# Optimization experiments

Hardware: AMD Instinct MI355X
Metric: run time of the kernel (lower is better)

## Reference

```python
import jax, jax.numpy as jnp
import numpy as np

ARITY, LABEL_DIM, H_DIM, B = 2, 128, 512, 16384
ARG_DIM = LABEL_DIM + ARITY * H_DIM


def setup_inputs() -> dict:
    key = jax.random.key(0)
    ks = jax.random.split(key, 12)
    s_lin = 1.0 / np.sqrt(ARG_DIM)
    inp = {
        "label": jax.random.normal(ks[0], (B, LABEL_DIM), jnp.float32),
        "children_h": jax.random.normal(ks[1], (ARITY, B, H_DIM), jnp.float32),
        "children_c": jax.random.normal(ks[2], (ARITY, B, H_DIM), jnp.float32),
        # torch Linear params: W (h, arg_dim), b (h,)
        "W_i": jax.random.normal(ks[3], (H_DIM, ARG_DIM), jnp.float32) * s_lin,
        "b_i": jax.random.normal(ks[4], (H_DIM,), jnp.float32) * s_lin,
        "W_o": jax.random.normal(ks[5], (H_DIM, ARG_DIM), jnp.float32) * s_lin,
        "b_o": jax.random.normal(ks[6], (H_DIM,), jnp.float32) * s_lin,
        "W_u": jax.random.normal(ks[7], (H_DIM, ARG_DIM), jnp.float32) * s_lin,
        "b_u": jax.random.normal(ks[8], (H_DIM,), jnp.float32) * s_lin,
        # forget params (xavier-ish init)
        "W_fl": jax.random.normal(ks[9], (H_DIM, LABEL_DIM), jnp.float32) * np.sqrt(2.0 / (H_DIM + LABEL_DIM)),
        "W_fs": jax.random.normal(ks[10], (ARITY, ARITY, H_DIM, H_DIM), jnp.float32) * np.sqrt(1.0 / H_DIM),
        "forget_bias": jax.random.normal(ks[11], (H_DIM,), jnp.float32) * 0.1,
    }
    return inp


def reference(label, children_h, children_c, W_i, b_i, W_o, b_o, W_u, b_u, W_fl, W_fs, forget_bias):
    arity, b, h = children_h.shape
    # x = cat([label, h_0, ..., h_{arity-1}], dim=1)  -> (B, arg_dim)
    x = jnp.concatenate([label, children_h.transpose(1, 0, 2).reshape(b, arity * h)], axis=1)
    i_gate = jax.nn.sigmoid(x @ W_i.T + b_i)
    o_gate = jax.nn.sigmoid(x @ W_o.T + b_o)
    u = jnp.tanh(x @ W_u.T + b_u)
    # per-child forget weight: [W_fl | W_fs[k,0] | ... | W_fs[k,arity-1]]  -> (arity, h, arg_dim)
    Wf = jnp.concatenate(
        [jnp.broadcast_to(W_fl, (arity,) + W_fl.shape),
         W_fs.transpose(0, 2, 1, 3).reshape(arity, h, arity * h)],
        axis=2,
    )
    # bmm (no bias inside sigmoid; forget_bias enters separately below)
    f = jax.nn.sigmoid(jnp.einsum("khd,bd->kbh", Wf, x))
    cells_composed = (f * children_c).sum(axis=0)          # (B, h)
    cells_forget_bias = forget_bias * children_c.sum(axis=0)
    next_cell = i_gate * u + cells_composed + cells_forget_bias
    out = jnp.tanh(o_gate * next_cell)
    return (next_cell, out)
```

## Files before the change

kernel.cpp:

```cpp
#include <hip/hip_runtime.h>
#include <hip/hip_bf16.h>
#include <cstdint>
#include <cstddef>

#define BROWS   16384
#define LDIM    128
#define HDIM    512
#define KDIM    1152
#define NGATES  2560
#define NKT     (KDIM / 64)

#define XB_BYTES  ((size_t)BROWS * KDIM * 2)
#define WB_BYTES  ((size_t)NGATES * KDIM * 2)

using f32x4   = __attribute__((ext_vector_type(4))) float;
using bfrag   = __attribute__((ext_vector_type(8))) short;

__device__ __forceinline__ short f2bf(float f) {
    union { float f; uint32_t u; } a; a.f = f;
    uint32_t u = a.u;
    uint32_t lsb = (u >> 16) & 1u;
    u += 0x7fffu + lsb;
    return (short)(u >> 16);
}

__device__ __forceinline__ void load_lds16(const void* g, void* l) {
    __builtin_amdgcn_global_load_lds(
        (const __attribute__((address_space(1))) void*)g,
        (__attribute__((address_space(3))) void*)l, 16, 0, 0);
}

__device__ __forceinline__ float fast_sigmoid(float x) {
    return 1.0f / (1.0f + __expf(-x));
}
__device__ __forceinline__ float fast_tanh(float x) {
    float t = __expf(2.0f * x);
    return 1.0f - 2.0f / (t + 1.0f);
}

#define NBX  ((BROWS  * (KDIM / 8)) / 256)
#define NBW  ((NGATES * (KDIM / 8)) / 256)

__global__ __launch_bounds__(256) void pack_all(
    const float* __restrict__ label, const float* __restrict__ chh,
    const float* __restrict__ Wi, const float* __restrict__ Wo,
    const float* __restrict__ Wu, const float* __restrict__ Wfl,
    const float* __restrict__ Wfs,
    short* __restrict__ xb, short* __restrict__ Wb)
{
    const int perRow = KDIM / 8;
    int blk = blockIdx.x;
    const float* src;
    short* dst;
    if (blk < NBX) {
        int tid = blk * 256 + threadIdx.x;
        int b = tid / perRow;
        int d = (tid - b * perRow) * 8;
        if (d < LDIM) {
            src = label + (size_t)b * LDIM + d;
        } else {
            int dd = d - LDIM;
            int k  = dd >> 9;
            int j  = dd & 511;
            src = chh + ((size_t)k * BROWS + b) * HDIM + j;
        }
        dst = xb + (size_t)b * KDIM + d;
    } else {
        int tid = (blk - NBX) * 256 + threadIdx.x;
        int n = tid / perRow;
        int d = (tid - n * perRow) * 8;
        int g = n >> 9, h = n & 511;
        if (g == 0)      src = Wi + (size_t)h * KDIM + d;
        else if (g == 1) src = Wo + (size_t)h * KDIM + d;
        else if (g == 2) src = Wu + (size_t)h * KDIM + d;
        else {
            int k = g - 3;
            if (d < LDIM) {
                src = Wfl + (size_t)h * LDIM + d;
            } else {
                int dd = d - LDIM;
                int j  = dd >> 9;
                int jj = dd & 511;
                src = Wfs + (((size_t)(k * 2 + j) * HDIM + h) * HDIM) + jj;
            }
        }
        dst = Wb + (size_t)n * KDIM + d;
    }
    float4 v0 = *(const float4*)src;
    float4 v1 = *(const float4*)(src + 4);
    bfrag s;
    s[0] = f2bf(v0.x); s[1] = f2bf(v0.y); s[2] = f2bf(v0.z); s[3] = f2bf(v0.w);
    s[4] = f2bf(v1.x); s[5] = f2bf(v1.y); s[6] = f2bf(v1.z); s[7] = f2bf(v1.w);
    *(bfrag*)dst = s;
}

__global__ __launch_bounds__(512, 2) void gemm_fused(
    const short* __restrict__ A, const short* __restrict__ Wb,
    const float* __restrict__ chc,
    const float* __restrict__ b_i, const float* __restrict__ b_o,
    const float* __restrict__ b_u, const float* __restrict__ fbias,
    float* __restrict__ out)
{
    __shared__ short As[2][16384];
    __shared__ short Bs[2][20480];

    const int t    = threadIdx.x;
    const int lane = t & 63;
    const int wave = t >> 6;
    const int wr   = wave >> 2;
    const int wc   = wave & 3;
    const int quad = lane >> 4;
    const int l16  = lane & 15;

    const int local = blockIdx.x >> 3;
    const int mT    = (blockIdx.x & 7) * 8 + (local >> 3);
    const int nT    = local & 7;
    const int mBase = mT * 256;
    const int h0    = nT * 64;

    f32x4 acc[8][5] = {};

    const int sr  = t >> 3;
    const int ssl = (t & 7) ^ (sr & 7);
    const short* aSrc = A  + (size_t)(mBase + sr) * KDIM + ssl * 8;
    const short* bSrc = Wb + (size_t)(h0    + sr) * KDIM + ssl * 8;
    short* aDst = &As[0][0] + t * 8;
    short* bDst = &Bs[0][0] + t * 8;

#define STAGE_A(q, kt, buf) load_lds16(aSrc + (size_t)(q) * (64 * KDIM) + (kt) * 64, \
                                       aDst + (buf) * 16384 + (q) * 4096)
#define STAGE_B(d, kt, buf) load_lds16(bSrc + (size_t)(d) * (512 * KDIM) + (kt) * 64, \
                                       bDst + (buf) * 20480 + (d) * 4096)

    const int kswz0 = ((quad)     ^ (l16 & 7)) << 4;
    const int kswz1 = ((quad + 4) ^ (l16 & 7)) << 4;
    const int aRowB = (wr * 128 + l16) << 7;
    const int bRowB = (wc * 16  + l16) << 7;

#define DS_A(buf, mh, i, ks) (*(const bfrag*)((const char*)(&As[0][0]) + (buf) * 32768 + \
                              aRowB + (mh) * 8192 + (i) * 2048 + ((ks) ? kswz1 : kswz0)))
#define DS_B(buf, g, ks) (*(const bfrag*)((const char*)(&Bs[0][0]) + (buf) * 40960 + \
                              (g) * 8192 + bRowB + ((ks) ? kswz1 : kswz0)))

#define MM(af, bfr, mi, g) acc[mi][g] = \
    __builtin_amdgcn_mfma_f32_16x16x32_bf16(af, bfr, acc[mi][g], 0, 0, 0)

#define PHASE(buf, mh, ks, ...) do { \
    bfrag a0 = DS_A(buf, mh, 0, ks); \
    bfrag a1 = DS_A(buf, mh, 1, ks); \
    bfrag a2 = DS_A(buf, mh, 2, ks); \
    bfrag a3 = DS_A(buf, mh, 3, ks); \
    bfrag b0 = DS_B(buf, 0, ks); \
    bfrag b1 = DS_B(buf, 1, ks); \
    bfrag b2 = DS_B(buf, 2, ks); \
    bfrag b3 = DS_B(buf, 3, ks); \
    bfrag b4 = DS_B(buf, 4, ks); \
    __VA_ARGS__; \
    __builtin_amdgcn_s_setprio(1); \
    MM(a0, b0, (mh)*4+0, 0); MM(a0, b1, (mh)*4+0, 1); MM(a0, b2, (mh)*4+0, 2); \
    MM(a0, b3, (mh)*4+0, 3); MM(a0, b4, (mh)*4+0, 4); \
    MM(a1, b0, (mh)*4+1, 0); MM(a1, b1, (mh)*4+1, 1); MM(a1, b2, (mh)*4+1, 2); \
    MM(a1, b3, (mh)*4+1, 3); MM(a1, b4, (mh)*4+1, 4); \
    MM(a2, b0, (mh)*4+2, 0); MM(a2, b1, (mh)*4+2, 1); MM(a2, b2, (mh)*4+2, 2); \
    MM(a2, b3, (mh)*4+2, 3); MM(a2, b4, (mh)*4+2, 4); \
    MM(a3, b0, (mh)*4+3, 0); MM(a3, b1, (mh)*4+3, 1); MM(a3, b2, (mh)*4+3, 2); \
    MM(a3, b3, (mh)*4+3, 3); MM(a3, b4, (mh)*4+3, 4); \
    __builtin_amdgcn_s_setprio(0); \
} while (0)

    STAGE_A(0, 0, 0); STAGE_A(1, 0, 0); STAGE_A(2, 0, 0); STAGE_A(3, 0, 0);
    STAGE_B(0, 0, 0); STAGE_B(1, 0, 0); STAGE_B(2, 0, 0); STAGE_B(3, 0, 0);
    STAGE_B(4, 0, 0);
    STAGE_A(0, 1, 1); STAGE_A(2, 1, 1);
    asm volatile("s_waitcnt vmcnt(2)" ::: "memory");
    __builtin_amdgcn_s_barrier();

#pragma unroll 1
    for (int k2 = 0; k2 < NKT / 2; ++k2) {
        const int kt   = 2 * k2;
        const bool more = (k2 < NKT / 2 - 1);

        PHASE(0, 0, 0, STAGE_A(1, kt + 1, 1); STAGE_B(0, kt + 1, 1); STAGE_B(1, kt + 1, 1));
        __builtin_amdgcn_s_barrier();
        PHASE(0, 0, 1, STAGE_A(3, kt + 1, 1); STAGE_B(2, kt + 1, 1); STAGE_B(3, kt + 1, 1));
        __builtin_amdgcn_s_barrier();
        PHASE(0, 1, 0, STAGE_B(4, kt + 1, 1); if (more) STAGE_A(0, kt + 2, 0));
        __builtin_amdgcn_s_barrier();
        PHASE(0, 1, 1, if (more) STAGE_A(2, kt + 2, 0));
        if (more) { asm volatile("s_waitcnt vmcnt(2)" ::: "memory"); }
        else      { asm volatile("s_waitcnt vmcnt(0)" ::: "memory"); }
        __builtin_amdgcn_s_barrier();

        PHASE(1, 0, 0, if (more) { STAGE_A(1, kt + 2, 0); STAGE_B(0, kt + 2, 0); STAGE_B(1, kt + 2, 0); });
        __builtin_amdgcn_s_barrier();
        PHASE(1, 0, 1, if (more) { STAGE_A(3, kt + 2, 0); STAGE_B(2, kt + 2, 0); STAGE_B(3, kt + 2, 0); });
        __builtin_amdgcn_s_barrier();
        PHASE(1, 1, 0, if (more) { STAGE_B(4, kt + 2, 0); STAGE_A(0, kt + 3, 1); });
        __builtin_amdgcn_s_barrier();
        PHASE(1, 1, 1, if (more) STAGE_A(2, kt + 3, 1));
        if (more) { asm volatile("s_waitcnt vmcnt(2)" ::: "memory"); }
        else      { asm volatile("s_waitcnt vmcnt(0)" ::: "memory"); }
        __builtin_amdgcn_s_barrier();
    }

    const int h = h0 + wc * 16 + l16;
    const float bi = b_i[h], bo = b_o[h], bu = b_u[h], fb = fbias[h];
    const float* chc1 = chc + (size_t)BROWS * HDIM;
    float* out2 = out + (size_t)BROWS * HDIM;

#pragma unroll
    for (int mi = 0; mi < 8; ++mi) {
        const int row0 = mBase + wr * 128 + mi * 16 + quad * 4;
#pragma unroll
        for (int r = 0; r < 4; ++r) {
            const size_t idx = (size_t)(row0 + r) * HDIM + h;
            float ig = fast_sigmoid(acc[mi][0][r] + bi);
            float og = fast_sigmoid(acc[mi][1][r] + bo);
            float uu = fast_tanh(acc[mi][2][r] + bu);
            float f0 = fast_sigmoid(acc[mi][3][r]);
            float f1 = fast_sigmoid(acc[mi][4][r]);
            float c0 = chc[idx];
            float c1 = chc1[idx];
            float ncell = ig * uu + f0 * c0 + f1 * c1 + fb * (c0 + c1);
            out[idx]  = ncell;
            out2[idx] = fast_tanh(og * ncell);
        }
    }
#undef PHASE
#undef MM
#undef DS_A
#undef DS_B
#undef STAGE_A
#undef STAGE_B
}

extern "C" void kernel_launch(void* const* d_in, const int* in_sizes, int n_in,
                              void* d_out, int out_size, void* d_ws, size_t ws_size,
                              hipStream_t stream) {
    const float* label = (const float*)d_in[0];
    const float* chh   = (const float*)d_in[1];
    const float* chc   = (const float*)d_in[2];
    const float* W_i   = (const float*)d_in[3];
    const float* b_i   = (const float*)d_in[4];
    const float* W_o   = (const float*)d_in[5];
    const float* b_o   = (const float*)d_in[6];
    const float* W_u   = (const float*)d_in[7];
    const float* b_u   = (const float*)d_in[8];
    const float* W_fl  = (const float*)d_in[9];
    const float* W_fs  = (const float*)d_in[10];
    const float* fbias = (const float*)d_in[11];
    float* out = (float*)d_out;

    char* ws = (char*)d_ws;
    short* xb = (short*)ws;
    short* Wb = (short*)(ws + XB_BYTES);

    pack_all<<<NBX + NBW, 256, 0, stream>>>(label, chh, W_i, W_o, W_u, W_fl, W_fs, xb, Wb);

    gemm_fused<<<dim3(512), 512, 0, stream>>>(xb, Wb, chc, b_i, b_o, b_u, fbias, out);
}
```

Baseline: 295.7 us.

## Replace phased GEMM pipeline with whole-tile double-buffered stage-and-compute loop

Replaces the 8-phase K-loop, which spread global-to-LDS loads across sub-phases with partial vmcnt waits and a barrier after each phase. Each K tile now issues all loads for the next tile into the other buffer at the start, runs all 80 MFMAs for the current tile in two k-halves, then waits for every load and takes one barrier. The aim is to cut barrier count and scheduling overhead. In exchange, loads are less finely interleaved with compute, and the full vmcnt(0) wait per tile may expose memory latency. More A fragments are also held live in registers at once.

```diff
diff --git a/kernel.cpp b/kernel.cpp
--- a/kernel.cpp
+++ b/kernel.cpp
@@ -131,77 +131,82 @@
                                        aDst + (buf) * 16384 + (q) * 4096)
 #define STAGE_B(d, kt, buf) load_lds16(bSrc + (size_t)(d) * (512 * KDIM) + (kt) * 64, \
                                        bDst + (buf) * 20480 + (d) * 4096)
+#define STAGE_ALL(kt, buf) do { \
+    STAGE_A(0, kt, buf); STAGE_A(1, kt, buf); STAGE_A(2, kt, buf); STAGE_A(3, kt, buf); \
+    STAGE_B(0, kt, buf); STAGE_B(1, kt, buf); STAGE_B(2, kt, buf); STAGE_B(3, kt, buf); \
+    STAGE_B(4, kt, buf); \
+} while (0)
 
     const int kswz0 = ((quad)     ^ (l16 & 7)) << 4;
     const int kswz1 = ((quad + 4) ^ (l16 & 7)) << 4;
     const int aRowB = (wr * 128 + l16) << 7;
     const int bRowB = (wc * 16  + l16) << 7;
 
-#define DS_A(buf, mh, i, ks) (*(const bfrag*)((const char*)(&As[0][0]) + (buf) * 32768 + \
-                              aRowB + (mh) * 8192 + (i) * 2048 + ((ks) ? kswz1 : kswz0)))
+#define DS_A(buf, mi, ks) (*(const bfrag*)((const char*)(&As[0][0]) + (buf) * 32768 + \
+                              aRowB + (mi) * 2048 + ((ks) ? kswz1 : kswz0)))
 #define DS_B(buf, g, ks) (*(const bfrag*)((const char*)(&Bs[0][0]) + (buf) * 40960 + \
                               (g) * 8192 + bRowB + ((ks) ? kswz1 : kswz0)))
 
 #define MM(af, bfr, mi, g) acc[mi][g] = \
     __builtin_amdgcn_mfma_f32_16x16x32_bf16(af, bfr, acc[mi][g], 0, 0, 0)
 
-#define PHASE(buf, mh, ks, ...) do { \
-    bfrag a0 = DS_A(buf, mh, 0, ks); \
-    bfrag a1 = DS_A(buf, mh, 1, ks); \
-    bfrag a2 = DS_A(buf, mh, 2, ks); \
-    bfrag a3 = DS_A(buf, mh, 3, ks); \
-    bfrag b0 = DS_B(buf, 0, ks); \
-    bfrag b1 = DS_B(buf, 1, ks); \
-    bfrag b2 = DS_B(buf, 2, ks); \
-    bfrag b3 = DS_B(buf, 3, ks); \
-    bfrag b4 = DS_B(buf, 4, ks); \
-    __VA_ARGS__; \
-    __builtin_amdgcn_s_setprio(1); \
-    MM(a0, b0, (mh)*4+0, 0); MM(a0, b1, (mh)*4+0, 1); MM(a0, b2, (mh)*4+0, 2); \
-    MM(a0, b3, (mh)*4+0, 3); MM(a0, b4, (mh)*4+0, 4); \
-    MM(a1, b0, (mh)*4+1, 0); MM(a1, b1, (mh)*4+1, 1); MM(a1, b2, (mh)*4+1, 2); \
-    MM(a1, b3, (mh)*4+1, 3); MM(a1, b4, (mh)*4+1, 4); \
-    MM(a2, b0, (mh)*4+2, 0); MM(a2, b1, (mh)*4+2, 1); MM(a2, b2, (mh)*4+2, 2); \
-    MM(a2, b3, (mh)*4+2, 3); MM(a2, b4, (mh)*4+2, 4); \
-    MM(a3, b0, (mh)*4+3, 0); MM(a3, b1, (mh)*4+3, 1); MM(a3, b2, (mh)*4+3, 2); \
-    MM(a3, b3, (mh)*4+3, 3); MM(a3, b4, (mh)*4+3, 4); \
-    __builtin_amdgcn_s_setprio(0); \
+#define TILE(bufc, kt, DOSTAGE, END) do { \
+    if (DOSTAGE) STAGE_ALL((kt) + 1, bufc ^ 1); \
+    { \
+        bfrag a0 = DS_A(bufc, 0, 0), a1 = DS_A(bufc, 1, 0); \
+        bfrag a2 = DS_A(bufc, 2, 0), a3 = DS_A(bufc, 3, 0); \
+        bfrag a4 = DS_A(bufc, 4, 0), a5 = DS_A(bufc, 5, 0); \
+        bfrag a6 = DS_A(bufc, 6, 0), a7 = DS_A(bufc, 7, 0); \
+        bfrag b0 = DS_B(bufc, 0, 0), b1 = DS_B(bufc, 1, 0); \
+        bfrag b2 = DS_B(bufc, 2, 0), b3 = DS_B(bufc, 3, 0); \
+        bfrag b4 = DS_B(bufc, 4, 0); \
+        __builtin_amdgcn_s_setprio(1); \
+        MM(a0, b0, 0, 0); MM(a0, b1, 0, 1); MM(a0, b2, 0, 2); MM(a0, b3, 0, 3); MM(a0, b4, 0, 4); \
+        MM(a1, b0, 1, 0); MM(a1, b1, 1, 1); MM(a1, b2, 1, 2); MM(a1, b3, 1, 3); MM(a1, b4, 1, 4); \
+        MM(a2, b0, 2, 0); MM(a2, b1, 2, 1); MM(a2, b2, 2, 2); MM(a2, b3, 2, 3); MM(a2, b4, 2, 4); \
+        MM(a3, b0, 3, 0); MM(a3, b1, 3, 1); MM(a3, b2, 3, 2); MM(a3, b3, 3, 3); MM(a3, b4, 3, 4); \
+        MM(a4, b0, 4, 0); MM(a4, b1, 4, 1); MM(a4, b2, 4, 2); MM(a4, b3, 4, 3); MM(a4, b4, 4, 4); \
+        MM(a5, b0, 5, 0); MM(a5, b1, 5, 1); MM(a5, b2, 5, 2); MM(a5, b3, 5, 3); MM(a5, b4, 5, 4); \
+        MM(a6, b0, 6, 0); MM(a6, b1, 6, 1); MM(a6, b2, 6, 2); MM(a6, b3, 6, 3); MM(a6, b4, 6, 4); \
+        MM(a7, b0, 7, 0); MM(a7, b1, 7, 1); MM(a7, b2, 7, 2); MM(a7, b3, 7, 3); MM(a7, b4, 7, 4); \
+        __builtin_amdgcn_s_setprio(0); \
+    } \
+    { \
+        bfrag a0 = DS_A(bufc, 0, 1), a1 = DS_A(bufc, 1, 1); \
+        bfrag a2 = DS_A(bufc, 2, 1), a3 = DS_A(bufc, 3, 1); \
+        bfrag a4 = DS_A(bufc, 4, 1), a5 = DS_A(bufc, 5, 1); \
+        bfrag a6 = DS_A(bufc, 6, 1), a7 = DS_A(bufc, 7, 1); \
+        bfrag b0 = DS_B(bufc, 0, 1), b1 = DS_B(bufc, 1, 1); \
+        bfrag b2 = DS_B(bufc, 2, 1), b3 = DS_B(bufc, 3, 1); \
+        bfrag b4 = DS_B(bufc, 4, 1); \
+        __builtin_amdgcn_s_setprio(1); \
+        MM(a0, b0, 0, 0); MM(a0, b1, 0, 1); MM(a0, b2, 0, 2); MM(a0, b3, 0, 3); MM(a0, b4, 0, 4); \
+        MM(a1, b0, 1, 0); MM(a1, b1, 1, 1); MM(a1, b2, 1, 2); MM(a1, b3, 1, 3); MM(a1, b4, 1, 4); \
+        MM(a2, b0, 2, 0); MM(a2, b1, 2, 1); MM(a2, b2, 2, 2); MM(a2, b3, 2, 3); MM(a2, b4, 2, 4); \
+        MM(a3, b0, 3, 0); MM(a3, b1, 3, 1); MM(a3, b2, 3, 2); MM(a3, b3, 3, 3); MM(a3, b4, 3, 4); \
+        MM(a4, b0, 4, 0); MM(a4, b1, 4, 1); MM(a4, b2, 4, 2); MM(a4, b3, 4, 3); MM(a4, b4, 4, 4); \
+        MM(a5, b0, 5, 0); MM(a5, b1, 5, 1); MM(a5, b2, 5, 2); MM(a5, b3, 5, 3); MM(a5, b4, 5, 4); \
+        MM(a6, b0, 6, 0); MM(a6, b1, 6, 1); MM(a6, b2, 6, 2); MM(a6, b3, 6, 3); MM(a6, b4, 6, 4); \
+        MM(a7, b0, 7, 0); MM(a7, b1, 7, 1); MM(a7, b2, 7, 2); MM(a7, b3, 7, 3); MM(a7, b4, 7, 4); \
+        __builtin_amdgcn_s_setprio(0); \
+    } \
+    if (END) { \
+        asm volatile("s_waitcnt vmcnt(0)" ::: "memory"); \
+        __builtin_amdgcn_s_barrier(); \
+    } \
 } while (0)
 
-    STAGE_A(0, 0, 0); STAGE_A(1, 0, 0); STAGE_A(2, 0, 0); STAGE_A(3, 0, 0);
-    STAGE_B(0, 0, 0); STAGE_B(1, 0, 0); STAGE_B(2, 0, 0); STAGE_B(3, 0, 0);
-    STAGE_B(4, 0, 0);
-    STAGE_A(0, 1, 1); STAGE_A(2, 1, 1);
-    asm volatile("s_waitcnt vmcnt(2)" ::: "memory");
+    STAGE_ALL(0, 0);
+    asm volatile("s_waitcnt vmcnt(0)" ::: "memory");
     __builtin_amdgcn_s_barrier();
 
 #pragma unroll 1
-    for (int k2 = 0; k2 < NKT / 2; ++k2) {
-        const int kt   = 2 * k2;
-        const bool more = (k2 < NKT / 2 - 1);
-
-        PHASE(0, 0, 0, STAGE_A(1, kt + 1, 1); STAGE_B(0, kt + 1, 1); STAGE_B(1, kt + 1, 1));
-        __builtin_amdgcn_s_barrier();
-        PHASE(0, 0, 1, STAGE_A(3, kt + 1, 1); STAGE_B(2, kt + 1, 1); STAGE_B(3, kt + 1, 1));
-        __builtin_amdgcn_s_barrier();
-        PHASE(0, 1, 0, STAGE_B(4, kt + 1, 1); if (more) STAGE_A(0, kt + 2, 0));
-        __builtin_amdgcn_s_barrier();
-        PHASE(0, 1, 1, if (more) STAGE_A(2, kt + 2, 0));
-        if (more) { asm volatile("s_waitcnt vmcnt(2)" ::: "memory"); }
-        else      { asm volatile("s_waitcnt vmcnt(0)" ::: "memory"); }
-        __builtin_amdgcn_s_barrier();
-
-        PHASE(1, 0, 0, if (more) { STAGE_A(1, kt + 2, 0); STAGE_B(0, kt + 2, 0); STAGE_B(1, kt + 2, 0); });
-        __builtin_amdgcn_s_barrier();
-        PHASE(1, 0, 1, if (more) { STAGE_A(3, kt + 2, 0); STAGE_B(2, kt + 2, 0); STAGE_B(3, kt + 2, 0); });
-        __builtin_amdgcn_s_barrier();
-        PHASE(1, 1, 0, if (more) { STAGE_B(4, kt + 2, 0); STAGE_A(0, kt + 3, 1); });
-        __builtin_amdgcn_s_barrier();
-        PHASE(1, 1, 1, if (more) STAGE_A(2, kt + 3, 1));
-        if (more) { asm volatile("s_waitcnt vmcnt(2)" ::: "memory"); }
-        else      { asm volatile("s_waitcnt vmcnt(0)" ::: "memory"); }
-        __builtin_amdgcn_s_barrier();
+    for (int k2 = 0; k2 < 8; ++k2) {
+        TILE(0, 2 * k2,     1, 1);
+        TILE(1, 2 * k2 + 1, 1, 1);
     }
+    TILE(0, 16, 1, 1);
+    TILE(1, 17, 0, 0);
 
     const int h = h0 + wc * 16 + l16;
     const float bi = b_i[h], bo = b_o[h], bu = b_u[h], fb = fbias[h];
@@ -226,10 +231,11 @@
             out2[idx] = fast_tanh(og * ncell);
         }
     }
-#undef PHASE
+#undef TILE
 #undef MM
 #undef DS_A
 #undef DS_B
+#undef STAGE_ALL
 #undef STAGE_A
 #undef STAGE_B
 }
```

New measurement: 284.3 us. -3.9%, faster.
